# Kernel tuning notes

Hardware: AMD Instinct MI355X
Metric: run time of the kernel (lower is better)

Reference implementation:

```python
import jax, jax.numpy as jnp
import numpy as np

N_HEAD = 16


def setup_inputs() -> dict:
    key = jax.random.key(0)
    k1, k2, k3 = jax.random.split(key, 3)
    B, T, C = 2, 2048, 1024
    x = jax.random.normal(k1, (B, T, C), dtype=jnp.float32)
    Wqkv = jax.random.normal(k2, (C, 3 * C), dtype=jnp.float32) * 0.02
    bqkv = jnp.zeros((3 * C,), dtype=jnp.float32)
    Wproj = jax.random.normal(k3, (C, C), dtype=jnp.float32) * 0.02
    bproj = jnp.zeros((C,), dtype=jnp.float32)
    return {"x": x, "Wqkv": Wqkv, "bqkv": bqkv, "Wproj": Wproj, "bproj": bproj}


def reference(x, Wqkv, bqkv, Wproj, bproj):
    b, t, c = x.shape
    h = N_HEAD
    d = c // h  # head_dim
    # qkv projection, split into q,k,v per head: (b,t,3,h,d)
    qkv = (x @ Wqkv + bqkv).reshape(b, t, 3, h, d)
    q, k, v = qkv[:, :, 0], qkv[:, :, 1], qkv[:, :, 2]  # each (b,t,h,d)
    # Faithful quirk of original: n_state = head_dim // heads, scale = 1/sqrt(n_state)
    scale = jnp.float32(1.0 / np.sqrt(d // h))
    # attn_mode == 'all': dense non-causal attention
    w = jnp.einsum('bqhd,bkhd->bhqk', q, k)  # (b,h,t,t)
    w = jax.nn.softmax(w * scale, axis=-1)
    a = jnp.einsum('bhqk,bkhd->bqhd', w, v).reshape(b, t, c)
    return a @ Wproj + bproj
```

## Files before the change

kernel.cpp:

```cpp
#include <hip/hip_runtime.h>

typedef float floatx4 __attribute__((ext_vector_type(4)));
typedef float floatx16 __attribute__((ext_vector_type(16)));
typedef __bf16 bf16x8 __attribute__((ext_vector_type(8)));
typedef __bf16 bf16x4 __attribute__((ext_vector_type(4)));
typedef __bf16 bf16x2 __attribute__((ext_vector_type(2)));
typedef float floatx2 __attribute__((ext_vector_type(2)));

#define MFMA16 __builtin_amdgcn_mfma_f32_16x16x32_bf16
#define MFMA32 __builtin_amdgcn_mfma_f32_32x32x16_bf16

typedef const __attribute__((address_space(1))) void* gas_t;
typedef __attribute__((address_space(3))) void* las_t;
#define GLD16(g, l) __builtin_amdgcn_global_load_lds((gas_t)(g), (las_t)(l), 16, 0, 0)

static __device__ __forceinline__ unsigned short f2bf(float f) {
  union { float f; unsigned int u; } v; v.f = f;
  unsigned int r = v.u + 0x7fffu + ((v.u >> 16) & 1u);
  return (unsigned short)(r >> 16);
}

static __device__ __forceinline__ unsigned pk2(float a, float b) {
  floatx2 v; v[0] = a; v[1] = b;
  union { bf16x2 h; unsigned u; } u;
  u.h = __builtin_convertvector(v, bf16x2);
  return u.u;
}

static __device__ __forceinline__ void cast_transpose_tile(
    const float* __restrict__ in, unsigned short* __restrict__ out,
    int R, int C, int bx, int by) {
  const int r0 = by * 64, c0 = bx * 64;
  const int tid = threadIdx.x;
  __shared__ float tl[64][65];
  const int rr = tid >> 4, cc = (tid & 15) * 4;
#pragma unroll
  for (int i = 0; i < 4; ++i) {
    int row = rr + i * 16;
    float4 v = *(const float4*)(in + (size_t)(r0 + row) * C + c0 + cc);
    tl[row][cc] = v.x; tl[row][cc + 1] = v.y;
    tl[row][cc + 2] = v.z; tl[row][cc + 3] = v.w;
  }
  __syncthreads();
  const int cl = tid >> 2, rbase = (tid & 3) * 16;
  unsigned short o[16];
#pragma unroll
  for (int j = 0; j < 16; ++j) o[j] = f2bf(tl[rbase + j][cl]);
  unsigned short* dst = out + (size_t)(c0 + cl) * R + r0 + rbase;
  *(uint4*)dst = *(uint4*)o;
  *(uint4*)(dst + 8) = *(uint4*)(o + 8);
}

__global__ __launch_bounds__(256) void prologue_kernel(
    const float* __restrict__ x, unsigned short* __restrict__ Xb,
    const float* __restrict__ Wqkv, unsigned short* __restrict__ Wqkvt,
    const float* __restrict__ Wproj, unsigned short* __restrict__ Wprojt) {
  const int bid = blockIdx.x;
  if (bid < 4096) {
    int i = bid * 256 + threadIdx.x;
    float4 v = ((const float4*)x)[i];
    ushort4 o;
    o.x = f2bf(v.x); o.y = f2bf(v.y); o.z = f2bf(v.z); o.w = f2bf(v.w);
    ((ushort4*)Xb)[i] = o;
  } else if (bid < 4096 + 768) {
    int b2 = bid - 4096;
    cast_transpose_tile(Wqkv, Wqkvt, 1024, 3072, b2 % 48, b2 / 48);
  } else {
    int b3 = bid - 4096 - 768;
    cast_transpose_tile(Wproj, Wprojt, 1024, 1024, b3 % 16, b3 / 16);
  }
}

__global__ __launch_bounds__(256) void gemm_qkv(
    const unsigned short* __restrict__ A,
    const unsigned short* __restrict__ Bt,
    const float* __restrict__ bias,
    unsigned short* __restrict__ Q,
    unsigned short* __restrict__ Kc,
    unsigned short* __restrict__ Vt) {
  const int K = 1024;
  const int m0 = blockIdx.y * 128, n0 = blockIdx.x * 128;
  const int tid = threadIdx.x, w = tid >> 6, l = tid & 63;
  const int l16 = l & 15, lq = l >> 4;
  const int wm = w >> 1, wn = w & 1;
  const int which = n0 >> 10;

  __shared__ __align__(16) unsigned short SH[32768];

  floatx4 acc[4][4] = {};

  int sA[4], sB[4];
  unsigned ldso[4];
#pragma unroll
  for (int j = 0; j < 4; ++j) {
    int s = j * 256 + tid;
    int row = s >> 3, blk = (s & 7) ^ (row & 7);
    sA[j] = (m0 + row) * K + blk * 8;
    sB[j] = (n0 + row) * K + blk * 8;
    ldso[j] = (unsigned)(j * 256 + w * 64) * 8;
  }

#pragma unroll
  for (int j = 0; j < 4; ++j) {
    GLD16(A + sA[j], SH + ldso[j]);
    GLD16(Bt + sB[j], SH + 8192 + ldso[j]);
  }

  if (which == 2) {
    for (int k0 = 0; k0 < K; k0 += 64) {
      __syncthreads();
      const int cur = (k0 >> 6) & 1;
      if (k0 + 64 < K) {
        const int nxt = cur ^ 1;
#pragma unroll
        for (int j = 0; j < 4; ++j) {
          GLD16(A + sA[j] + k0 + 64, SH + nxt * 16384 + ldso[j]);
          GLD16(Bt + sB[j] + k0 + 64, SH + nxt * 16384 + 8192 + ldso[j]);
        }
      }
      const unsigned short* As = SH + cur * 16384;
      const unsigned short* Bs = SH + cur * 16384 + 8192;
#pragma unroll
      for (int kk = 0; kk < 2; ++kk) {
        bf16x8 af[4], bf[4];
#pragma unroll
        for (int mi = 0; mi < 4; ++mi) {
          int row = wm * 64 + mi * 16 + l16;
          int blk = (kk * 4 + lq) ^ (l16 & 7);
          af[mi] = *(const bf16x8*)(As + row * 64 + blk * 8);
        }
#pragma unroll
        for (int ni = 0; ni < 4; ++ni) {
          int row = wn * 64 + ni * 16 + l16;
          int blk = (kk * 4 + lq) ^ (l16 & 7);
          bf[ni] = *(const bf16x8*)(Bs + row * 64 + blk * 8);
        }
#pragma unroll
        for (int ni = 0; ni < 4; ++ni)
#pragma unroll
          for (int mi = 0; mi < 4; ++mi)
            acc[mi][ni] = MFMA16(af[mi], bf[ni], acc[mi][ni], 0, 0, 0);
      }
    }
    float bv[4];
#pragma unroll
    for (int ni = 0; ni < 4; ++ni) bv[ni] = bias[n0 + wn * 64 + ni * 16 + l16];
    __syncthreads();
    unsigned short* E = SH + w * 2304;
    const int bh = (m0 >> 11) * 16 + ((n0 & 1023) >> 6) + wn;
    const int tt0 = (m0 & 2047) + wm * 64;
    const int m8 = l & 7, bc = 16 * (m8 >> 1) + 4 * (m8 & 1);
#pragma unroll
    for (int p = 0; p < 2; ++p) {
#pragma unroll
      for (int n2 = 0; n2 < 2; ++n2) {
        int ni = p * 2 + n2;
#pragma unroll
        for (int mi = 0; mi < 4; ++mi) {
          floatx4 vv = acc[mi][ni] + bv[ni];
          *(bf16x4*)(E + (n2 * 16 + l16) * 72 + mi * 16 + lq * 4) =
              __builtin_convertvector(vv, bf16x4);
        }
      }
#pragma unroll
      for (int s = 0; s < 4; ++s) {
        int dl = s * 8 + (l >> 3);
        union { bf16x4 h[2]; bf16x8 v; } uu;
        uu.h[0] = *(const bf16x4*)(E + dl * 72 + bc);
        uu.h[1] = *(const bf16x4*)(E + dl * 72 + bc + 8);
        *(bf16x8*)(Vt + ((size_t)bh * 64 + p * 32 + dl) * 2048 + tt0 +
                   m8 * 8) = uu.v;
      }
    }
  } else {
    for (int k0 = 0; k0 < K; k0 += 64) {
      __syncthreads();
      const int cur = (k0 >> 6) & 1;
      if (k0 + 64 < K) {
        const int nxt = cur ^ 1;
#pragma unroll
        for (int j = 0; j < 4; ++j) {
          GLD16(A + sA[j] + k0 + 64, SH + nxt * 16384 + ldso[j]);
          GLD16(Bt + sB[j] + k0 + 64, SH + nxt * 16384 + 8192 + ldso[j]);
        }
      }
      const unsigned short* As = SH + cur * 16384;
      const unsigned short* Bs = SH + cur * 16384 + 8192;
#pragma unroll
      for (int kk = 0; kk < 2; ++kk) {
        bf16x8 af[4], bf[4];
#pragma unroll
        for (int mi = 0; mi < 4; ++mi) {
          int row = wm * 64 + mi * 16 + l16;
          int blk = (kk * 4 + lq) ^ (l16 & 7);
          af[mi] = *(const bf16x8*)(As + row * 64 + blk * 8);
        }
#pragma unroll
        for (int ni = 0; ni < 4; ++ni) {
          int row = wn * 64 + ni * 16 + l16;
          int blk = (kk * 4 + lq) ^ (l16 & 7);
          bf[ni] = *(const bf16x8*)(Bs + row * 64 + blk * 8);
        }
#pragma unroll
        for (int ni = 0; ni < 4; ++ni)
#pragma unroll
          for (int mi = 0; mi < 4; ++mi)
            acc[mi][ni] = MFMA16(bf[ni], af[mi], acc[mi][ni], 0, 0, 0);
      }
    }
    const float sc = (which == 0) ? 0.7213475204444817f : 1.0f;
    unsigned short* dst = (which == 0) ? Q : Kc;
    __syncthreads();
    unsigned short* E = SH + w * 2304;
    const int bh = (m0 >> 11) * 16 + ((n0 & 1023) >> 6) + wn;
    const size_t gbase = ((size_t)bh * 2048 + (m0 & 2047) + wm * 64) * 64;
#pragma unroll
    for (int p = 0; p < 2; ++p) {
#pragma unroll
      for (int m2 = 0; m2 < 2; ++m2) {
        int mi = p * 2 + m2;
#pragma unroll
        for (int ni = 0; ni < 4; ++ni) {
          int col0 = n0 + wn * 64 + ni * 16 + lq * 4;
          floatx4 bv = *(const floatx4*)(bias + col0);
          floatx4 vv = (acc[mi][ni] + bv) * sc;
          *(bf16x4*)(E + (m2 * 16 + l16) * 72 + ni * 16 + lq * 4) =
              __builtin_convertvector(vv, bf16x4);
        }
      }
#pragma unroll
      for (int s = 0; s < 4; ++s) {
        int rl = s * 8 + (l >> 3);
        bf16x8 vv = *(const bf16x8*)(E + rl * 72 + (l & 7) * 8);
        *(bf16x8*)(dst + gbase + (size_t)(p * 32 + rl) * 64 + (l & 7) * 8) =
            vv;
      }
    }
  }
}

__global__ __launch_bounds__(256, 2) void attn_kernel(
    const unsigned short* __restrict__ Q,
    const unsigned short* __restrict__ Kc,
    const unsigned short* __restrict__ Vt,
    unsigned short* __restrict__ AO) {
  const int T = 2048;
  const int bid = blockIdx.x;
  const int lin = (bid & 7) * 64 + (bid >> 3);
  const int bh = lin >> 4, q0 = (lin & 15) * 128;
  const int tid = threadIdx.x, w = tid >> 6, l = tid & 63;
  const int r31 = l & 31, g = l >> 5;
  const int kh = w >> 1, wq = w & 1;

  __shared__ __align__(16) float oex[128 * 68];
  __shared__ float Lex[256];

  bf16x8 qf[2][4];
#pragma unroll
  for (int qt = 0; qt < 2; ++qt) {
    const unsigned short* qr =
        Q + ((size_t)bh * T + q0 + wq * 64 + qt * 32 + r31) * 64 + g * 8;
#pragma unroll
    for (int ds = 0; ds < 4; ++ds) qf[qt][ds] = *(const bf16x8*)(qr + ds * 16);
  }

  floatx16 o_acc[2][2] = {};
  float l_lane[2] = {0.f, 0.f};

  const unsigned short* kbase =
      Kc + ((size_t)bh * T + kh * 1024) * 64 + (size_t)r31 * 64 + g * 8;
  const unsigned short* vbase =
      Vt + ((size_t)bh * 64 + r31) * T + kh * 1024 + g * 8;

  for (int c = 0; c < 16; ++c) {
    const unsigned short* kc = kbase + c * 64 * 64;
    bf16x8 kf[2][4];
#pragma unroll
    for (int kt = 0; kt < 2; ++kt)
#pragma unroll
      for (int ds = 0; ds < 4; ++ds)
        kf[kt][ds] = *(const bf16x8*)(kc + kt * 32 * 64 + ds * 16);

    const unsigned short* vc = vbase + c * 64;
    bf16x8 vf[2][4];
#pragma unroll
    for (int dt = 0; dt < 2; ++dt)
#pragma unroll
      for (int s = 0; s < 4; ++s)
        vf[dt][s] = *(const bf16x8*)(vc + (size_t)dt * 32 * T + s * 16);

    bf16x8 pf[2][4];
#pragma unroll
    for (int qt = 0; qt < 2; ++qt) {
#pragma unroll
      for (int kt = 0; kt < 2; ++kt) {
        floatx16 z = {};
#pragma unroll
        for (int ds = 0; ds < 4; ++ds)
          z = MFMA32(kf[kt][ds], qf[qt][ds], z, 0, 0, 0);

        float pe[16];
#pragma unroll
        for (int r = 0; r < 16; ++r) pe[r] = __builtin_amdgcn_exp2f(z[r]);
        l_lane[qt] += (((pe[0] + pe[1]) + (pe[2] + pe[3])) +
                       ((pe[4] + pe[5]) + (pe[6] + pe[7]))) +
                      (((pe[8] + pe[9]) + (pe[10] + pe[11])) +
                       ((pe[12] + pe[13]) + (pe[14] + pe[15])));
#pragma unroll
        for (int s2 = 0; s2 < 2; ++s2) {
          union { unsigned u[4]; bf16x8 v; } pu;
          pu.u[0] = pk2(pe[8 * s2 + 0], pe[8 * s2 + 1]);
          pu.u[1] = pk2(pe[8 * s2 + 2], pe[8 * s2 + 3]);
          pu.u[2] = pk2(pe[8 * s2 + 4], pe[8 * s2 + 5]);
          pu.u[3] = pk2(pe[8 * s2 + 6], pe[8 * s2 + 7]);
          pf[qt][kt * 2 + s2] = pu.v;
        }
      }
    }

#pragma unroll
    for (int dt = 0; dt < 2; ++dt)
#pragma unroll
      for (int s = 0; s < 4; ++s)
#pragma unroll
        for (int qt = 0; qt < 2; ++qt)
          o_acc[qt][dt] = MFMA32(vf[dt][s], pf[qt][s], o_acc[qt][dt], 0, 0, 0);
  }

  __syncthreads();
  if (kh == 1) {
    float* r = oex + (wq * 64 + l) * 68;
#pragma unroll
    for (int qt = 0; qt < 2; ++qt) {
#pragma unroll
      for (int dt = 0; dt < 2; ++dt)
#pragma unroll
        for (int rq = 0; rq < 4; ++rq) {
          floatx4 ov;
          ov[0] = o_acc[qt][dt][rq * 4 + 0];
          ov[1] = o_acc[qt][dt][rq * 4 + 1];
          ov[2] = o_acc[qt][dt][rq * 4 + 2];
          ov[3] = o_acc[qt][dt][rq * 4 + 3];
          *(floatx4*)(r + qt * 32 + dt * 16 + rq * 4) = ov;
        }
      Lex[(wq * 64 + l) * 2 + qt] = l_lane[qt];
    }
  }
  __syncthreads();
  if (kh == 0) {
    const float* r = oex + (wq * 64 + l) * 68;
    const int b = bh >> 4, h = bh & 15;
#pragma unroll
    for (int qt = 0; qt < 2; ++qt) {
      float ls = l_lane[qt] + Lex[(wq * 64 + l) * 2 + qt];
      ls += __shfl_xor(ls, 32, 64);
      float inv = 1.0f / ls;
      const int t = q0 + wq * 64 + qt * 32 + r31;
      unsigned short* ao = AO + ((size_t)b * 2048 + t) * 1024 + h * 64;
#pragma unroll
      for (int dt = 0; dt < 2; ++dt)
#pragma unroll
        for (int rq = 0; rq < 4; ++rq) {
          floatx4 ov;
          ov[0] = o_acc[qt][dt][rq * 4 + 0];
          ov[1] = o_acc[qt][dt][rq * 4 + 1];
          ov[2] = o_acc[qt][dt][rq * 4 + 2];
          ov[3] = o_acc[qt][dt][rq * 4 + 3];
          ov += *(const floatx4*)(r + qt * 32 + dt * 16 + rq * 4);
          ov *= inv;
          *(bf16x4*)(ao + dt * 32 + rq * 8 + g * 4) =
              __builtin_convertvector(ov, bf16x4);
        }
    }
  }
}

__global__ __launch_bounds__(256) void gemm_proj(
    const unsigned short* __restrict__ A,
    const unsigned short* __restrict__ Bt,
    const float* __restrict__ bias,
    float* __restrict__ out) {
  const int K = 1024, N = 1024;
  const int m0 = blockIdx.y * 128, n0 = blockIdx.x * 64;
  const int tid = threadIdx.x, w = tid >> 6, l = tid & 63;
  const int l16 = l & 15, lq = l >> 4;

  __shared__ __align__(16) unsigned short SH[24576];

  floatx4 acc[2][4] = {};

  int sA[4], sB[2];
  unsigned ldsoA[4], ldsoB[2];
#pragma unroll
  for (int j = 0; j < 4; ++j) {
    int s = j * 256 + tid;
    int row = s >> 3, blk = (s & 7) ^ (row & 7);
    sA[j] = (m0 + row) * K + blk * 8;
    ldsoA[j] = (unsigned)(j * 256 + w * 64) * 8;
  }
#pragma unroll
  for (int j = 0; j < 2; ++j) {
    int s = j * 256 + tid;
    int row = s >> 3, blk = (s & 7) ^ (row & 7);
    sB[j] = (n0 + row) * K + blk * 8;
    ldsoB[j] = (unsigned)(j * 256 + w * 64) * 8;
  }

#pragma unroll
  for (int j = 0; j < 4; ++j) GLD16(A + sA[j], SH + ldsoA[j]);
#pragma unroll
  for (int j = 0; j < 2; ++j) GLD16(Bt + sB[j], SH + 8192 + ldsoB[j]);

  for (int k0 = 0; k0 < K; k0 += 64) {
    __syncthreads();
    const int cur = (k0 >> 6) & 1;
    if (k0 + 64 < K) {
      const int nxt = cur ^ 1;
#pragma unroll
      for (int j = 0; j < 4; ++j)
        GLD16(A + sA[j] + k0 + 64, SH + nxt * 12288 + ldsoA[j]);
#pragma unroll
      for (int j = 0; j < 2; ++j)
        GLD16(Bt + sB[j] + k0 + 64, SH + nxt * 12288 + 8192 + ldsoB[j]);
    }
    const unsigned short* As = SH + cur * 12288;
    const unsigned short* Bs = SH + cur * 12288 + 8192;
#pragma unroll
    for (int kk = 0; kk < 2; ++kk) {
      bf16x8 af[2], bf[4];
#pragma unroll
      for (int mi = 0; mi < 2; ++mi) {
        int row = w * 32 + mi * 16 + l16;
        int blk = (kk * 4 + lq) ^ (l16 & 7);
        af[mi] = *(const bf16x8*)(As + row * 64 + blk * 8);
      }
#pragma unroll
      for (int ni = 0; ni < 4; ++ni) {
        int row = ni * 16 + l16;
        int blk = (kk * 4 + lq) ^ (l16 & 7);
        bf[ni] = *(const bf16x8*)(Bs + row * 64 + blk * 8);
      }
#pragma unroll
      for (int ni = 0; ni < 4; ++ni)
#pragma unroll
        for (int mi = 0; mi < 2; ++mi)
          acc[mi][ni] = MFMA16(bf[ni], af[mi], acc[mi][ni], 0, 0, 0);
    }
  }

#pragma unroll
  for (int mi = 0; mi < 2; ++mi) {
    int t = m0 + w * 32 + mi * 16 + l16;
#pragma unroll
    for (int ni = 0; ni < 4; ++ni) {
      int col0 = n0 + ni * 16 + lq * 4;
      floatx4 bv = *(const floatx4*)(bias + col0);
      *(floatx4*)(out + (size_t)t * N + col0) = acc[mi][ni] + bv;
    }
  }
}

extern "C" void kernel_launch(void* const* d_in, const int* in_sizes, int n_in,
                              void* d_out, int out_size, void* d_ws,
                              size_t ws_size, hipStream_t stream) {
  const float* x     = (const float*)d_in[0];
  const float* Wqkv  = (const float*)d_in[1];
  const float* bqkv  = (const float*)d_in[2];
  const float* Wproj = (const float*)d_in[3];
  const float* bproj = (const float*)d_in[4];
  float* out = (float*)d_out;

  unsigned short* Xb     = (unsigned short*)d_ws;
  unsigned short* Wqkvt  = Xb + 4194304;
  unsigned short* Wprojt = Wqkvt + 3145728;
  unsigned short* Qb     = Wprojt + 1048576;
  unsigned short* Kb     = Qb + 4194304;
  unsigned short* Vtb    = Kb + 4194304;
  unsigned short* AOb    = Vtb + 4194304;

  prologue_kernel<<<5120, 256, 0, stream>>>(x, Xb, Wqkv, Wqkvt, Wproj, Wprojt);
  gemm_qkv<<<dim3(24, 32), 256, 0, stream>>>(Xb, Wqkvt, bqkv, Qb, Kb, Vtb);
  attn_kernel<<<512, 256, 0, stream>>>(Qb, Kb, Vtb, AOb);
  gemm_proj<<<dim3(16, 32), 256, 0, stream>>>(AOb, Wprojt, bproj, out);
}
```

Measured before the change: 191.8 us.

## Stage K/V through swizzled LDS double buffer and split keys over 8 waves

The attention kernel now uses 512 threads and splits the keys into four 512-key quarters instead of two halves. Each quarter's K and V tiles are async-copied into double-buffered, XOR-swizzled LDS with global_load_lds, so the fetch of the next tile overlaps compute on the current one. Per-wave fragments now come from LDS instead of direct global loads. The partial sums are reduced in two rounds through a shared buffer of about 70KB, which adds block-wide syncs and LDS pressure that could cap occupancy.

```diff
diff --git a/kernel.cpp b/kernel.cpp
--- a/kernel.cpp
+++ b/kernel.cpp
@@ -239,7 +239,7 @@
   }
 }
 
-__global__ __launch_bounds__(256, 2) void attn_kernel(
+__global__ __launch_bounds__(512, 4) void attn_kernel(
     const unsigned short* __restrict__ Q,
     const unsigned short* __restrict__ Kc,
     const unsigned short* __restrict__ Vt,
@@ -248,12 +248,16 @@
   const int bid = blockIdx.x;
   const int lin = (bid & 7) * 64 + (bid >> 3);
   const int bh = lin >> 4, q0 = (lin & 15) * 128;
-  const int tid = threadIdx.x, w = tid >> 6, l = tid & 63;
+  const int tid = threadIdx.x, l = tid & 63;
   const int r31 = l & 31, g = l >> 5;
-  const int kh = w >> 1, wq = w & 1;
-
-  __shared__ __align__(16) float oex[128 * 68];
-  __shared__ float Lex[256];
+  const int kh = tid >> 7;
+  const int wq = (tid >> 6) & 1;
+  const int h128 = tid & 127;
+
+  __shared__ __align__(16) char SHB[71680];
+  unsigned short* KV = (unsigned short*)SHB;
+  float* oex = (float*)SHB;
+  float* Lex = oex + 256 * 68;
 
   bf16x8 qf[2][4];
 #pragma unroll
@@ -267,66 +271,126 @@
   floatx16 o_acc[2][2] = {};
   float l_lane[2] = {0.f, 0.f};
 
-  const unsigned short* kbase =
-      Kc + ((size_t)bh * T + kh * 1024) * 64 + (size_t)r31 * 64 + g * 8;
-  const unsigned short* vbase =
-      Vt + ((size_t)bh * 64 + r31) * T + kh * 1024 + g * 8;
-
-  for (int c = 0; c < 16; ++c) {
-    const unsigned short* kc = kbase + c * 64 * 64;
-    bf16x8 kf[2][4];
-#pragma unroll
-    for (int kt = 0; kt < 2; ++kt)
+  const unsigned short* kbase = Kc + ((size_t)bh * T + kh * 512) * 64;
+  const unsigned short* vbase = Vt + (size_t)bh * 64 * T + kh * 512;
+
+  int kro[2], vro[2];
+  unsigned ldsK[2], ldsV[2];
+#pragma unroll
+  for (int j = 0; j < 2; ++j) {
+    int s = j * 128 + h128;
+    int rK = s >> 3;
+    kro[j] = rK * 64 + (((s & 7) ^ (rK & 7)) << 3);
+    int rV = s >> 2;
+    vro[j] = rV * T + (((s & 3) ^ (rV & 3)) << 3);
+    ldsK[j] = (unsigned)(j * 128 + (h128 & 64)) * 8;
+    ldsV[j] = ldsK[j] + 2048;
+  }
+  unsigned short* myKV = KV + kh * 8192;
+
+#define STAGE(c, b)                                                  \
+  {                                                                  \
+    _Pragma("unroll") for (int j = 0; j < 2; ++j) {                  \
+      GLD16(kbase + (c) * 2048 + kro[j], myKV + (b) * 4096 + ldsK[j]); \
+      GLD16(vbase + (c) * 32 + vro[j], myKV + (b) * 4096 + ldsV[j]);   \
+    }                                                                \
+  }
+
+  STAGE(0, 0);
+
+  for (int it = 0; it < 16; ++it) {
+    __syncthreads();
+    if (it < 15) STAGE(it + 1, (it + 1) & 1);
+    const unsigned short* kb = myKV + (it & 1) * 4096;
+    const unsigned short* vb = kb + 2048;
+
+    bf16x8 kf[4];
+    {
+      const int rx = r31 & 7;
+      const unsigned short* kr = kb + r31 * 64;
 #pragma unroll
       for (int ds = 0; ds < 4; ++ds)
-        kf[kt][ds] = *(const bf16x8*)(kc + kt * 32 * 64 + ds * 16);
-
-    const unsigned short* vc = vbase + c * 64;
-    bf16x8 vf[2][4];
-#pragma unroll
-    for (int dt = 0; dt < 2; ++dt)
-#pragma unroll
-      for (int s = 0; s < 4; ++s)
-        vf[dt][s] = *(const bf16x8*)(vc + (size_t)dt * 32 * T + s * 16);
-
-    bf16x8 pf[2][4];
+        kf[ds] = *(const bf16x8*)(kr + (((ds * 2 + g) ^ rx) << 3));
+    }
+
+    bf16x8 pf[2][2];
 #pragma unroll
     for (int qt = 0; qt < 2; ++qt) {
-#pragma unroll
-      for (int kt = 0; kt < 2; ++kt) {
-        floatx16 z = {};
-#pragma unroll
-        for (int ds = 0; ds < 4; ++ds)
-          z = MFMA32(kf[kt][ds], qf[qt][ds], z, 0, 0, 0);
-
-        float pe[16];
-#pragma unroll
-        for (int r = 0; r < 16; ++r) pe[r] = __builtin_amdgcn_exp2f(z[r]);
-        l_lane[qt] += (((pe[0] + pe[1]) + (pe[2] + pe[3])) +
-                       ((pe[4] + pe[5]) + (pe[6] + pe[7]))) +
-                      (((pe[8] + pe[9]) + (pe[10] + pe[11])) +
-                       ((pe[12] + pe[13]) + (pe[14] + pe[15])));
-#pragma unroll
-        for (int s2 = 0; s2 < 2; ++s2) {
-          union { unsigned u[4]; bf16x8 v; } pu;
-          pu.u[0] = pk2(pe[8 * s2 + 0], pe[8 * s2 + 1]);
-          pu.u[1] = pk2(pe[8 * s2 + 2], pe[8 * s2 + 3]);
-          pu.u[2] = pk2(pe[8 * s2 + 4], pe[8 * s2 + 5]);
-          pu.u[3] = pk2(pe[8 * s2 + 6], pe[8 * s2 + 7]);
-          pf[qt][kt * 2 + s2] = pu.v;
-        }
-      }
-    }
-
-#pragma unroll
-    for (int dt = 0; dt < 2; ++dt)
-#pragma unroll
-      for (int s = 0; s < 4; ++s)
+      floatx16 z = {};
+#pragma unroll
+      for (int ds = 0; ds < 4; ++ds)
+        z = MFMA32(kf[ds], qf[qt][ds], z, 0, 0, 0);
+
+      float pe[16];
+#pragma unroll
+      for (int r = 0; r < 16; ++r) pe[r] = __builtin_amdgcn_exp2f(z[r]);
+      l_lane[qt] += (((pe[0] + pe[1]) + (pe[2] + pe[3])) +
+                     ((pe[4] + pe[5]) + (pe[6] + pe[7]))) +
+                    (((pe[8] + pe[9]) + (pe[10] + pe[11])) +
+                     ((pe[12] + pe[13]) + (pe[14] + pe[15])));
+#pragma unroll
+      for (int s2 = 0; s2 < 2; ++s2) {
+        union { unsigned u[4]; bf16x8 v; } pu;
+        pu.u[0] = pk2(pe[8 * s2 + 0], pe[8 * s2 + 1]);
+        pu.u[1] = pk2(pe[8 * s2 + 2], pe[8 * s2 + 3]);
+        pu.u[2] = pk2(pe[8 * s2 + 4], pe[8 * s2 + 5]);
+        pu.u[3] = pk2(pe[8 * s2 + 6], pe[8 * s2 + 7]);
+        pf[qt][s2] = pu.v;
+      }
+    }
+
+#pragma unroll
+    for (int dt = 0; dt < 2; ++dt) {
+      const int row = dt * 32 + r31, rx4 = row & 3;
+      const unsigned short* vr = vb + row * 32;
+#pragma unroll
+      for (int s = 0; s < 2; ++s) {
+        bf16x8 vf = *(const bf16x8*)(vr + (((s * 2 + g) ^ rx4) << 3));
 #pragma unroll
         for (int qt = 0; qt < 2; ++qt)
-          o_acc[qt][dt] = MFMA32(vf[dt][s], pf[qt][s], o_acc[qt][dt], 0, 0, 0);
-  }
-
+          o_acc[qt][dt] = MFMA32(vf, pf[qt][s], o_acc[qt][dt], 0, 0, 0);
+      }
+    }
+  }
+#undef STAGE
+
+  __syncthreads();
+  if (kh >= 2) {
+    float* r = oex + ((kh & 1) * 128 + wq * 64 + l) * 68;
+#pragma unroll
+    for (int qt = 0; qt < 2; ++qt) {
+#pragma unroll
+      for (int dt = 0; dt < 2; ++dt)
+#pragma unroll
+        for (int rq = 0; rq < 4; ++rq) {
+          floatx4 ov;
+          ov[0] = o_acc[qt][dt][rq * 4 + 0];
+          ov[1] = o_acc[qt][dt][rq * 4 + 1];
+          ov[2] = o_acc[qt][dt][rq * 4 + 2];
+          ov[3] = o_acc[qt][dt][rq * 4 + 3];
+          *(floatx4*)(r + qt * 32 + dt * 16 + rq * 4) = ov;
+        }
+      Lex[((kh & 1) * 128 + wq * 64 + l) * 2 + qt] = l_lane[qt];
+    }
+  }
+  __syncthreads();
+  if (kh < 2) {
+    const float* r = oex + (kh * 128 + wq * 64 + l) * 68;
+#pragma unroll
+    for (int qt = 0; qt < 2; ++qt) {
+#pragma unroll
+      for (int dt = 0; dt < 2; ++dt)
+#pragma unroll
+        for (int rq = 0; rq < 4; ++rq) {
+          floatx4 pv = *(const floatx4*)(r + qt * 32 + dt * 16 + rq * 4);
+          o_acc[qt][dt][rq * 4 + 0] += pv[0];
+          o_acc[qt][dt][rq * 4 + 1] += pv[1];
+          o_acc[qt][dt][rq * 4 + 2] += pv[2];
+          o_acc[qt][dt][rq * 4 + 3] += pv[3];
+        }
+      l_lane[qt] += Lex[(kh * 128 + wq * 64 + l) * 2 + qt];
+    }
+  }
   __syncthreads();
   if (kh == 1) {
     float* r = oex + (wq * 64 + l) * 68;
@@ -480,6 +544,6 @@
 
   prologue_kernel<<<5120, 256, 0, stream>>>(x, Xb, Wqkv, Wqkvt, Wproj, Wprojt);
   gemm_qkv<<<dim3(24, 32), 256, 0, stream>>>(Xb, Wqkvt, bqkv, Qb, Kb, Vtb);
-  attn_kernel<<<512, 256, 0, stream>>>(Qb, Kb, Vtb, AOb);
+  attn_kernel<<<512, 512, 0, stream>>>(Qb, Kb, Vtb, AOb);
   gemm_proj<<<dim3(16, 32), 256, 0, stream>>>(AOb, Wprojt, bproj, out);
 }
```

Measured after the change: 252.8 us. +31.8%, slower.
